# Optimization experiments

Hardware: AMD Instinct MI355X
Metric: run time of the kernel (lower is better)

Reference implementation:

```python
import jax, jax.numpy as jnp
import numpy as np

T, B, I, H = 2048, 64, 256, 256


def setup_inputs() -> dict:
    key = jax.random.key(0)
    ks = jax.random.split(key, 5)
    s = 1.0 / np.sqrt(H)
    return {
        "x": jax.random.normal(ks[0], (T, B, I), jnp.float32),
        "h0": jnp.zeros((B, H), jnp.float32),
        "c0": jnp.zeros((B, H), jnp.float32),
        "W_i": jax.random.uniform(ks[1], (4 * H, I), jnp.float32, -s, s),
        "W_h": jax.random.uniform(ks[2], (4 * H, H), jnp.float32, -s, s),
        "b_i": jax.random.uniform(ks[3], (4 * H,), jnp.float32, -s, s),
        "b_h": jax.random.uniform(ks[4], (4 * H,), jnp.float32, -s, s),
    }


def reference(x, h0, c0, W_i, W_h, b_i, b_h):
    # Precompute the input projection for all timesteps in one big GEMM:
    # [T,B,I] @ [I,4H] -> [T,B,4H]
    xproj = jnp.einsum("tbi,gi->tbg", x, W_i) + (b_i + b_h)

    def step(carry, xg):
        h, c = carry
        # subLSTM: all four gates are sigmoid. Gate order: in, out, z, forget.
        gates = jax.nn.sigmoid(xg + h @ W_h.T)  # [B,4H]
        i_g, o_g, z_g, f_g = jnp.split(gates, 4, axis=-1)
        c_new = c * f_g + z_g - i_g
        h_new = jax.nn.sigmoid(c_new) - o_g
        return (h_new, c_new), h_new

    (h_T, c_T), outputs = jax.lax.scan(step, (h0, c0), xproj)
    return outputs, (h_T, c_T)
```

## Files before the change

kernel.cpp:

```cpp
#include <hip/hip_runtime.h>


typedef __attribute__((ext_vector_type(4))) float f32x4;
typedef __attribute__((ext_vector_type(8))) short bf16x8;
typedef __attribute__((ext_vector_type(4))) int i32x4;
typedef __attribute__((ext_vector_type(4))) unsigned short u16x4;

constexpr float WSCALE = 2032.0f;
constexpr float SC = 1.0f / (2032.0f * 127.0f);

__device__ __forceinline__ unsigned short f2bf(float f) {
  unsigned u = __builtin_bit_cast(unsigned, f);
  u += 0x7fffu + ((u >> 16) & 1u);
  return (unsigned short)(u >> 16);
}
__device__ __forceinline__ float sigmf(float x) {
  return __builtin_amdgcn_rcpf(1.0f + __expf(-x));
}

__global__ void quantw_kernel(const float* __restrict__ Wh,
                              signed char* __restrict__ Wq) {
  int i = blockIdx.x * 256 + threadIdx.x;
  float q = rintf(Wh[i] * WSCALE);
  q = fminf(127.0f, fmaxf(-127.0f, q));
  Wq[i] = (signed char)(int)q;
}

__device__ __forceinline__ void gemm_body(char* smem, int gb,
                                          const float* __restrict__ x,
                                          const float* __restrict__ Wi,
                                          const float* __restrict__ bi,
                                          const float* __restrict__ bh,
                                          float* __restrict__ xpOut, long m0) {
  typedef unsigned short row72[72];
  row72* Al = (row72*)smem;
  row72* Bl = (row72*)(smem + 18432);
  const int tid = threadIdx.x;
  const int act = tid < 256;
  const int lane = tid & 63, wv = (tid >> 6) & 3;
  const int wm = wv >> 1, wn = wv & 1, cl = lane & 15, cg = lane >> 4;
  const int bx = gb >> 3, by = gb & 7;
  const long gm0 = m0 + (long)bx * 128;
  const int lm0 = bx * 128;
  const int n0 = by * 128;
  const int srow = (tid & 255) >> 1, sh = (tid & 1) * 32;

  f32x4 acc[4][4];
#pragma unroll
  for (int m = 0; m < 4; ++m)
#pragma unroll
    for (int n = 0; n < 4; ++n) acc[m][n] = (f32x4){0.f, 0.f, 0.f, 0.f};

  for (int kt = 0; kt < 4; ++kt) {
    if (act) {
      const float* pa = x + (gm0 + srow) * 256 + kt * 64 + sh;
      const float* pb = Wi + (long)(n0 + srow) * 256 + kt * 64 + sh;
#pragma unroll
      for (int j = 0; j < 8; ++j) {
        f32x4 va = *(const f32x4*)(pa + j * 4);
        f32x4 vb = *(const f32x4*)(pb + j * 4);
        u16x4 ua, ub;
#pragma unroll
        for (int k = 0; k < 4; ++k) { ua[k] = f2bf(va[k]); ub[k] = f2bf(vb[k]); }
        *(u16x4*)&Al[srow][sh + j * 4] = ua;
        *(u16x4*)&Bl[srow][sh + j * 4] = ub;
      }
    }
    __syncthreads();
    if (act) {
#pragma unroll
      for (int ks = 0; ks < 2; ++ks) {
        bf16x8 af[4], bfv[4];
#pragma unroll
        for (int m = 0; m < 4; ++m)
          af[m] = *(const bf16x8*)&Al[wm * 64 + m * 16 + cl][ks * 32 + cg * 8];
#pragma unroll
        for (int n = 0; n < 4; ++n)
          bfv[n] = *(const bf16x8*)&Bl[wn * 64 + n * 16 + cl][ks * 32 + cg * 8];
#pragma unroll
        for (int m = 0; m < 4; ++m)
#pragma unroll
          for (int n = 0; n < 4; ++n)
            acc[m][n] = __builtin_amdgcn_mfma_f32_16x16x32_bf16(
                af[m], bfv[n], acc[m][n], 0, 0, 0);
      }
    }
    __syncthreads();
  }
  if (act) {
#pragma unroll
    for (int n = 0; n < 4; ++n) {
      int gn = n0 + wn * 64 + n * 16 + cl;
      float bias = bi[gn] + bh[gn];
#pragma unroll
      for (int m = 0; m < 4; ++m) {
        int lrow = lm0 + wm * 64 + m * 16 + cg * 4;
#pragma unroll
        for (int r = 0; r < 4; ++r)
          xpOut[(long)(lrow + r) * 1024 + gn] = acc[m][n][r] + bias;
      }
    }
  }
}

#define SB() __builtin_amdgcn_sched_barrier(0)

#define RAW_BARRIER()                                         \
  do {                                                        \
    __builtin_amdgcn_sched_barrier(0);                        \
    asm volatile("s_waitcnt lgkmcnt(0)" ::: "memory");        \
    __builtin_amdgcn_s_barrier();                             \
    asm volatile("" ::: "memory");                            \
    __builtin_amdgcn_sched_barrier(0);                        \
  } while (0)

#define MFMA16G_BODY(A0_, A1_, A2_, A3_, TG, HEAD)                            \
  asm volatile(HEAD                                                           \
               "v_mfma_i32_16x16x64_i8 %0, %20, %4, %24\n\t"                  \
               "v_mfma_i32_16x16x64_i8 %1, %20, %5, %24\n\t"                  \
               "v_mfma_i32_16x16x64_i8 %2, %20, %6, %24\n\t"                  \
               "v_mfma_i32_16x16x64_i8 %3, %20, %7, %24\n\t"                  \
               "v_mfma_i32_16x16x64_i8 %0, %21, %8, %0\n\t"                   \
               "v_mfma_i32_16x16x64_i8 %1, %21, %9, %1\n\t"                   \
               "v_mfma_i32_16x16x64_i8 %2, %21, %10, %2\n\t"                  \
               "v_mfma_i32_16x16x64_i8 %3, %21, %11, %3\n\t"                  \
               "v_mfma_i32_16x16x64_i8 %0, %22, %12, %0\n\t"                  \
               "v_mfma_i32_16x16x64_i8 %1, %22, %13, %1\n\t"                  \
               "v_mfma_i32_16x16x64_i8 %2, %22, %14, %2\n\t"                  \
               "v_mfma_i32_16x16x64_i8 %3, %22, %15, %3\n\t"                  \
               "v_mfma_i32_16x16x64_i8 %0, %23, %16, %0\n\t"                  \
               "v_mfma_i32_16x16x64_i8 %1, %23, %17, %1\n\t"                  \
               "v_mfma_i32_16x16x64_i8 %2, %23, %18, %2\n\t"                  \
               "v_mfma_i32_16x16x64_i8 %3, %23, %19, %3"                      \
               : "=&v"(A0_), "=&v"(A1_), "=&v"(A2_), "=&v"(A3_)               \
               : "a"(wf[TG][0][0]), "a"(wf[TG][1][0]), "a"(wf[TG][2][0]),     \
                 "a"(wf[TG][3][0]), "a"(wf[TG][0][1]), "a"(wf[TG][1][1]),     \
                 "a"(wf[TG][2][1]), "a"(wf[TG][3][1]), "a"(wf[TG][0][2]),     \
                 "a"(wf[TG][1][2]), "a"(wf[TG][2][2]), "a"(wf[TG][3][2]),     \
                 "a"(wf[TG][0][3]), "a"(wf[TG][1][3]), "a"(wf[TG][2][3]),     \
                 "a"(wf[TG][3][3]), "v"(bq0), "v"(bq1), "v"(bq2), "v"(bq3),   \
                 "v"(zq))

#define MFMA16G1(A0_, A1_, A2_, A3_, TG) \
  MFMA16G_BODY(A0_, A1_, A2_, A3_, TG, "s_nop 3\n\t")
#define MFMA16G(A0_, A1_, A2_, A3_, TG) \
  MFMA16G_BODY(A0_, A1_, A2_, A3_, TG, "")

#define SEL4(A0_, A1_, A2_, A3_)                 \
  ({                                             \
    int lo_ = cg0_ ? (A1_)[0] : (A0_)[0];        \
    int hi_ = cg0_ ? (A3_)[0] : (A2_)[0];        \
    cg1_ ? hi_ : lo_;                            \
  })

#define STEP(TT, XBUF)                                                         \
  do {                                                                         \
    const int rs = (TT) & 1;                                                   \
    i32x4 bq0 = *(const i32x4*)((const char*)(&hq[rs][0]) + 0 + cg * 16);      \
    i32x4 bq1 = *(const i32x4*)((const char*)(&hq[rs][0]) + 64 + cg * 16);     \
    i32x4 bq2 = *(const i32x4*)((const char*)(&hq[rs][0]) + 128 + cg * 16);    \
    i32x4 bq3 = *(const i32x4*)((const char*)(&hq[rs][0]) + 192 + cg * 16);    \
    if ((TT) > 0)                    \
      out[((long)(t0 + (TT)-1) * 64 + b) * 256 + u] = hv_p;                    \
    float x3s_ = XBUF[3], x2s_ = XBUF[2], x1s_ = XBUF[1], x0s_ = XBUF[0];      \
    if ((TT) + 2 < nt) {       \
      _Pragma("unroll") for (int tg = 0; tg < 4; ++tg)                         \
          XBUF[tg] = xp[((long)((TT) + 2) * 64 + b) * 1024 + tg * 256 + u];    \
    }                                                                          \
    i32x4 aF0, aF1, aF2, aF3, aZ0, aZ1, aZ2, aZ3;                              \
    i32x4 aI0, aI1, aI2, aI3, aO0, aO1, aO2, aO3;                              \
    SB();                                                                      \
    MFMA16G1(aF0, aF1, aF2, aF3, 3);                               \
    MFMA16G(aZ0, aZ1, aZ2, aZ3, 2);                                \
    MFMA16G(aI0, aI1, aI2, aI3, 0);                                \
    MFMA16G(aO0, aO1, aO2, aO3, 1);                                \
    SB();                                                                      \
    float gf = sigmf(x3s_ + SC * (float)SEL4(aF0, aF1, aF2, aF3));             \
    float gz = sigmf(x2s_ + SC * (float)SEL4(aZ0, aZ1, aZ2, aZ3));             \
    float gi = sigmf(x0s_ + SC * (float)SEL4(aI0, aI1, aI2, aI3));             \
    c_own = c_own * gf + gz - gi;                                              \
    float sc_ = sigmf(c_own);                                                  \
    float go = sigmf(x1s_ + SC * (float)SEL4(aO0, aO1, aO2, aO3));             \
    float hv = sc_ - go;                                                       \
    int qv = (int)rintf(hv * 127.0f);                                          \
    ((signed char*)(&hq[rs ^ 1][0]))[u] = (signed char)qv;                     \
    hv_p = hv;                                                                 \
    RAW_BARRIER();                                                             \
  } while (0)

__device__ __forceinline__ void recur_body(
    char* smem, const float* __restrict__ xp, float* __restrict__ out,
    float* __restrict__ cst, int* __restrict__ hqst,
    const float* __restrict__ h0, const float* __restrict__ c0,
    const signed char* __restrict__ Wq, int t0, int nt, int first, int last) {
  const int b = blockIdx.x, tid = threadIdx.x;
  const int w = tid >> 6, lane = tid & 63, cl = lane & 15, cg = lane >> 4;
  const int cg0_ = cg & 1, cg1_ = (cg >> 1) & 1;
  const int u = w * 64 + cg * 16 + cl;
  int(*hq)[64] = (int(*)[64])smem;

  i32x4 wf[4][4][4];
#pragma unroll
  for (int tg = 0; tg < 4; ++tg)
#pragma unroll
    for (int j = 0; j < 4; ++j)
#pragma unroll
      for (int q = 0; q < 4; ++q)
        wf[tg][j][q] =
            *(const i32x4*)(Wq + (tg * 256 + w * 64 + j * 16 + cl) * 256 +
                            q * 64 + cg * 16);

  const i32x4 zq = {0, 0, 0, 0};

  float c_own = first ? c0[b * 256 + u] : cst[b * 256 + u];
  float hv_p = 0.0f;

  if (tid < 64) {
    int word;
    if (first) {
      int qj[4];
#pragma unroll
      for (int j = 0; j < 4; ++j) {
        float v = h0[b * 256 + tid * 4 + j];
        qj[j] = (int)rintf(fminf(1.0f, fmaxf(-1.0f, v)) * 127.0f);
      }
      word = (qj[0] & 255) | ((qj[1] & 255) << 8) | ((qj[2] & 255) << 16) |
             ((qj[3] & 255) << 24);
    } else {
      word = hqst[b * 64 + tid];
    }
    hq[0][tid] = word;
  }

  float xa[4], xb[4];
#pragma unroll
  for (int tg = 0; tg < 4; ++tg) {
    xa[tg] = xp[((long)0 * 64 + b) * 1024 + tg * 256 + u];
    xb[tg] = xp[((long)1 * 64 + b) * 1024 + tg * 256 + u];
  }
  __syncthreads();

  for (int t = 0; t < nt; t += 2) {
    STEP(t, xa);
    STEP(t + 1, xb);
  }

  out[((long)(t0 + nt - 1) * 64 + b) * 256 + u] = hv_p;
  if (last) {
    out[33554432L + b * 256 + u] = hv_p;
    out[33554432L + 16384L + b * 256 + u] = c_own;
  }
  cst[b * 256 + u] = c_own;
  if (tid < 64) hqst[b * 64 + tid] = hq[0][tid];
}

__global__ __launch_bounds__(256, 1) void fused_kernel(
    const float* __restrict__ x, const float* __restrict__ Wi,
    const float* __restrict__ bi, const float* __restrict__ bh,
    float* __restrict__ gslot, long m0, int have_gemm,
    const float* __restrict__ rslot, float* __restrict__ out,
    float* __restrict__ cst, int* __restrict__ hqst,
    const float* __restrict__ h0, const float* __restrict__ c0,
    const signed char* __restrict__ Wq, int t0, int nt, int first, int last,
    int have_recur) {
  __shared__ __align__(16) char smem[83968];
  if (blockIdx.x < 64) {
    if (have_recur)
      recur_body(smem, rslot, out, cst, hqst, h0, c0, Wq, t0, nt, first, last);
  } else {
    if (have_gemm) gemm_body(smem, blockIdx.x - 64, x, Wi, bi, bh, gslot, m0);
  }
}

extern "C" void kernel_launch(void* const* d_in, const int* in_sizes, int n_in,
                              void* d_out, int out_size, void* d_ws,
                              size_t ws_size, hipStream_t stream) {
  const float* x = (const float*)d_in[0];
  const float* h0 = (const float*)d_in[1];
  const float* c0 = (const float*)d_in[2];
  const float* Wi = (const float*)d_in[3];
  const float* Wh = (const float*)d_in[4];
  const float* bi = (const float*)d_in[5];
  const float* bh = (const float*)d_in[6];
  float* out = (float*)d_out;

  const size_t fixed = 262144  + 65536  + 16384 ;
  int chunkT = 32;
  const int cands[4] = {256, 128, 64, 32};
  for (int i = 0; i < 4; ++i) {
    size_t slot = (size_t)cands[i] * 64 * 1024 * 4;
    if (fixed + 2 * slot <= ws_size) { chunkT = cands[i]; break; }
  }

  char* p = (char*)d_ws;
  signed char* Wq = (signed char*)p;  p += 262144;
  float* cst = (float*)p;             p += 65536;
  int* hqst = (int*)p;                p += 16384;
  float* ring = (float*)p;
  const size_t slotElems = (size_t)chunkT * 64 * 1024;

  quantw_kernel<<<1024, 256, 0, stream>>>(Wh, Wq);

  const int nchunks = 2048 / chunkT;
  for (int c = 0; c <= nchunks; ++c) {
    const int hg = (c < nchunks) ? 1 : 0;
    const int hr = (c > 0) ? 1 : 0;
    float* gs = ring + (size_t)(c & 1) * slotElems;
    const float* rs = ring + (size_t)((c ^ 1) & 1) * slotElems;
    const int ngb = hg ? (chunkT / 2) * 8 : 0;
    fused_kernel<<<64 + ngb, 256, 0, stream>>>(
        x, Wi, bi, bh, gs, (long)c * chunkT * 64, hg, rs, out, cst, hqst, h0,
        c0, Wq, (c - 1) * chunkT, chunkT, (c == 1) ? 1 : 0,
        (c == nchunks) ? 1 : 0, hr);
  }
}
```

Baseline: 1.540 ms.

## Fold -log2e into precomputed projection and use exp2 gates with 4-deep x prefetch

```diff
diff --git a/kernel.cpp b/kernel.cpp
--- a/kernel.cpp
+++ b/kernel.cpp
@@ -8,14 +8,13 @@
 
 constexpr float WSCALE = 2032.0f;
 constexpr float SC = 1.0f / (2032.0f * 127.0f);
+constexpr float NEGL2E = -1.44269504f;
+constexpr float MSCL2E = SC * NEGL2E;
 
 __device__ __forceinline__ unsigned short f2bf(float f) {
   unsigned u = __builtin_bit_cast(unsigned, f);
   u += 0x7fffu + ((u >> 16) & 1u);
   return (unsigned short)(u >> 16);
-}
-__device__ __forceinline__ float sigmf(float x) {
-  return __builtin_amdgcn_rcpf(1.0f + __expf(-x));
 }
 
 __global__ void quantw_kernel(const float* __restrict__ Wh,
@@ -97,7 +96,7 @@
         int lrow = lm0 + wm * 64 + m * 16 + cg * 4;
 #pragma unroll
         for (int r = 0; r < 4; ++r)
-          xpOut[(long)(lrow + r) * 1024 + gn] = acc[m][n][r] + bias;
+          xpOut[(long)(lrow + r) * 1024 + gn] = (acc[m][n][r] + bias) * NEGL2E;
       }
     }
   }
@@ -114,9 +113,8 @@
     __builtin_amdgcn_sched_barrier(0);                        \
   } while (0)
 
-#define MFMA16G_BODY(A0_, A1_, A2_, A3_, TG, HEAD)                            \
-  asm volatile(HEAD                                                           \
-               "v_mfma_i32_16x16x64_i8 %0, %20, %4, %24\n\t"                  \
+#define MFMA16G(A0_, A1_, A2_, A3_, TG)                                       \
+  asm volatile("v_mfma_i32_16x16x64_i8 %0, %20, %4, %24\n\t"                  \
                "v_mfma_i32_16x16x64_i8 %1, %20, %5, %24\n\t"                  \
                "v_mfma_i32_16x16x64_i8 %2, %20, %6, %24\n\t"                  \
                "v_mfma_i32_16x16x64_i8 %3, %20, %7, %24\n\t"                  \
@@ -141,11 +139,6 @@
                  "a"(wf[TG][3][3]), "v"(bq0), "v"(bq1), "v"(bq2), "v"(bq3),   \
                  "v"(zq))
 
-#define MFMA16G1(A0_, A1_, A2_, A3_, TG) \
-  MFMA16G_BODY(A0_, A1_, A2_, A3_, TG, "s_nop 3\n\t")
-#define MFMA16G(A0_, A1_, A2_, A3_, TG) \
-  MFMA16G_BODY(A0_, A1_, A2_, A3_, TG, "")
-
 #define SEL4(A0_, A1_, A2_, A3_)                 \
   ({                                             \
     int lo_ = cg0_ ? (A1_)[0] : (A0_)[0];        \
@@ -153,7 +146,10 @@
     cg1_ ? hi_ : lo_;                            \
   })
 
-#define STEP(TT, XBUF)                                                         \
+#define GATE(FV_, XN_) \
+  __builtin_amdgcn_rcpf(1.0f + exp2f(fmaf((FV_), MSCL2E, (XN_))))
+
+#define STEP(TT, XBUF, XB2)                                                    \
   do {                                                                         \
     const int rs = (TT) & 1;                                                   \
     i32x4 bq0 = *(const i32x4*)((const char*)(&hq[rs][0]) + 0 + cg * 16);      \
@@ -162,25 +158,24 @@
     i32x4 bq3 = *(const i32x4*)((const char*)(&hq[rs][0]) + 192 + cg * 16);    \
     if ((TT) > 0)                    \
       out[((long)(t0 + (TT)-1) * 64 + b) * 256 + u] = hv_p;                    \
-    float x3s_ = XBUF[3], x2s_ = XBUF[2], x1s_ = XBUF[1], x0s_ = XBUF[0];      \
     if ((TT) + 2 < nt) {       \
       _Pragma("unroll") for (int tg = 0; tg < 4; ++tg)                         \
-          XBUF[tg] = xp[((long)((TT) + 2) * 64 + b) * 1024 + tg * 256 + u];    \
+          XB2[tg] = xp[((long)((TT) + 2) * 64 + b) * 1024 + tg * 256 + u];     \
     }                                                                          \
     i32x4 aF0, aF1, aF2, aF3, aZ0, aZ1, aZ2, aZ3;                              \
     i32x4 aI0, aI1, aI2, aI3, aO0, aO1, aO2, aO3;                              \
     SB();                                                                      \
-    MFMA16G1(aF0, aF1, aF2, aF3, 3);                               \
+    MFMA16G(aF0, aF1, aF2, aF3, 3);                                \
     MFMA16G(aZ0, aZ1, aZ2, aZ3, 2);                                \
     MFMA16G(aI0, aI1, aI2, aI3, 0);                                \
     MFMA16G(aO0, aO1, aO2, aO3, 1);                                \
     SB();                                                                      \
-    float gf = sigmf(x3s_ + SC * (float)SEL4(aF0, aF1, aF2, aF3));             \
-    float gz = sigmf(x2s_ + SC * (float)SEL4(aZ0, aZ1, aZ2, aZ3));             \
-    float gi = sigmf(x0s_ + SC * (float)SEL4(aI0, aI1, aI2, aI3));             \
+    float gf = GATE((float)SEL4(aF0, aF1, aF2, aF3), XBUF[3]);                 \
+    float gz = GATE((float)SEL4(aZ0, aZ1, aZ2, aZ3), XBUF[2]);                 \
+    float gi = GATE((float)SEL4(aI0, aI1, aI2, aI3), XBUF[0]);                 \
     c_own = c_own * gf + gz - gi;                                              \
-    float sc_ = sigmf(c_own);                                                  \
-    float go = sigmf(x1s_ + SC * (float)SEL4(aO0, aO1, aO2, aO3));             \
+    float sc_ = __builtin_amdgcn_rcpf(1.0f + exp2f(c_own * NEGL2E));           \
+    float go = GATE((float)SEL4(aO0, aO1, aO2, aO3), XBUF[1]);                 \
     float hv = sc_ - go;                                                       \
     int qv = (int)rintf(hv * 127.0f);                                          \
     ((signed char*)(&hq[rs ^ 1][0]))[u] = (signed char)qv;                     \
@@ -232,7 +227,7 @@
     hq[0][tid] = word;
   }
 
-  float xa[4], xb[4];
+  float xa[4], xb[4], xc[4], xd[4];
 #pragma unroll
   for (int tg = 0; tg < 4; ++tg) {
     xa[tg] = xp[((long)0 * 64 + b) * 1024 + tg * 256 + u];
@@ -240,9 +235,11 @@
   }
   __syncthreads();
 
-  for (int t = 0; t < nt; t += 2) {
-    STEP(t, xa);
-    STEP(t + 1, xb);
+  for (int t = 0; t < nt; t += 4) {
+    STEP(t, xa, xc);
+    STEP(t + 1, xb, xd);
+    STEP(t + 2, xc, xa);
+    STEP(t + 3, xd, xb);
   }
 
   out[((long)(t0 + nt - 1) * 64 + b) * 256 + u] = hv_p;
```

New measurement: 1.544 ms. No clear change (+0.3%).
